# Performance work log

Hardware: AMD Instinct MI355X
Metric: run time of the kernel (lower is better)

Reference implementation:

```python
import jax, jax.numpy as jnp
import numpy as np

TK = 3          # number of temporal scales (wavedec level = TK-1)
SK = 3          # spatial rank count per scale (SK-1 rank-1 terms + residual)
INPUT_LEN = 256
N_NODES = 256
K = 32          # randomized-SVD sketch size
INV_SQRT2 = np.float32(1.0 / np.sqrt(2.0))


def haar_wavedec(x, levels):
    # x: (..., L) with L divisible by 2**levels; pywt haar, mode='zero', even L
    # returns [cD1, cD2, ..., cD_levels, cA_levels]  (== pywt.wavedec(...)[::-1])
    coeffs = []
    for _ in range(levels):
        L = x.shape[-1]
        pairs = x.reshape(x.shape[:-1] + (L // 2, 2))
        a, b = pairs[..., 0], pairs[..., 1]
        coeffs.append((a - b) * INV_SQRT2)  # detail cD
        x = (a + b) * INV_SQRT2             # approx cA
    coeffs.append(x)
    return coeffs


def setup_inputs() -> dict:
    key = jax.random.key(0)
    kx, kp = jax.random.split(key)
    x = jax.random.normal(kx, (4, INPUT_LEN, 64, N_NODES), dtype=jnp.float32)
    p = jax.random.normal(kp, (N_NODES, K), dtype=jnp.float32)
    return {"x": x, "p": p}


def reference(x, p):
    # x: (B, T, c, n) -> permute(0,2,3,1) -> (B, c, n, T)
    xw = jnp.transpose(x, (0, 2, 3, 1))
    coeffs = haar_wavedec(xw, TK - 1)  # TK tensors (B, c, n, L_i)
    res = []
    for xi in coeffs:
        if SK == 1:
            res.append(xi)
            continue
        xt = jnp.transpose(xi, (0, 3, 1, 2))          # (B, L, c, n)
        z = xt @ p                                     # (B, L, c, k)
        q, _ = jnp.linalg.qr(z)                        # reduced: (B, L, c, k)
        y = jnp.einsum('blck,blcn->blkn', q, xt)       # (B, L, k, n)
        u, s, vh = jnp.linalg.svd(y, full_matrices=False)  # u:(B,L,k,k) s:(B,L,k) vh:(B,L,k,n)
        u = q @ u                                      # (B, L, c, k)
        # rank-1 terms s_j * u_j v_j^T for j < SK-1, vectorized over j
        terms = jnp.einsum('blcj,blj,bljn->jblcn',
                           u[..., :SK - 1], s[..., :SK - 1], vh[..., :SK - 1, :])
        terms = jnp.transpose(terms, (0, 1, 3, 4, 2))  # (SK-1, B, c, n, L)
        resid = xi - terms.sum(axis=0)
        for j in range(SK - 1):
            res.append(terms[j])
        res.append(resid)
    # left-pad last dim to INPUT_LEN, then stack -> (TK*SK, B, c, n, INPUT_LEN)
    res = [jnp.pad(r, ((0, 0), (0, 0), (0, 0), (INPUT_LEN - r.shape[-1], 0))) for r in res]
    return jnp.stack(res)
```

## Files before the change

### kernel.cpp

```cpp
#include <hip/hip_runtime.h>

#define IS2f 0.70710678118654752440f

#define WS_Z   0ul
#define WS_G   2097152ul
#define WS_H   3145728ul
#define WS_SU  4194304ul
#define WS_VV  4325376ul
#define WS_B   4849664ul

#define WSYNC() asm volatile("" ::: "memory")

__device__ __forceinline__ float frcp(float v){ return __builtin_amdgcn_rcpf(v); }
__device__ __forceinline__ float frsq(float v){ return __builtin_amdgcn_rsqf(v); }
__device__ __forceinline__ float fsq (float v){ return __builtin_amdgcn_sqrtf(v); }
__device__ __forceinline__ float readlane_f(float v, int sl){
  return __uint_as_float(__builtin_amdgcn_readlane(__float_as_uint(v), sl));
}

__device__ __forceinline__ void decode_pid(int pid, int& ci, int& b, int& l, int& L){
  if (pid < 512)      { ci = 0; b = pid >> 7; l = pid & 127; L = 128; }
  else if (pid < 768) { int q = pid - 512; ci = 1; b = q >> 6; l = q & 63; L = 64; }
  else                { int q = pid - 768; ci = 2; b = q >> 6; l = q & 63; L = 64; }
}
__device__ __forceinline__ int su_base(int ci){ return ci==0 ? 0 : (ci==1 ? 65536 : 98304); }
__device__ __forceinline__ int vv_base(int ci){ return ci==0 ? 0 : (ci==1 ? 262144 : 393216); }
__device__ __forceinline__ int tpp(int r, int m){ return (m==0) ? r  : (r+m)%31; }
__device__ __forceinline__ int tqq(int r, int m){ return (m==0) ? 31 : (r+31-m)%31; }

#define PTS 260

__global__ __launch_bounds__(512) void k_fact(const float* __restrict__ x,
                                              const float* __restrict__ p,
                                              float* __restrict__ ws, int storeB){
  __shared__ __align__(16) float Ms[64*256];
  __shared__ __align__(16) float Zs[64*32];
  __shared__ __align__(16) float Pt[32*PTS];
  __shared__ __align__(16) float Bn[32*PTS];

  int pid = blockIdx.x, tid = threadIdx.x;
  int ci,b,l,L; decode_pid(pid,ci,b,l,L);

  {
    const float4* p4 = (const float4*)p;
    #pragma unroll
    for (int e=0;e<4;++e){
      int idx = tid + 512*e;
      int n = idx >> 3, k4 = idx & 7;
      float4 v = p4[idx];
      Pt[(4*k4+0)*PTS + n] = v.x;
      Pt[(4*k4+1)*PTS + n] = v.y;
      Pt[(4*k4+2)*PTS + n] = v.z;
      Pt[(4*k4+3)*PTS + n] = v.w;
    }
  }
  const float4* x4 = (const float4*)x;
  float4* Ms4 = (float4*)Ms;
  if (ci == 0){
    size_t base = ((size_t)(b*256 + 2*l) * 64) * 64;
    #pragma unroll
    for (int e=0;e<8;++e){
      int f = tid + 512*e;
      float4 A = x4[base + f];
      float4 Bv = x4[base + 4096 + f];
      float4 m;
      m.x=(A.x-Bv.x)*IS2f; m.y=(A.y-Bv.y)*IS2f; m.z=(A.z-Bv.z)*IS2f; m.w=(A.w-Bv.w)*IS2f;
      Ms4[f] = m;
    }
  } else {
    float sg = (ci==1) ? -0.5f : 0.5f;
    size_t base = ((size_t)(b*256 + 4*l) * 64) * 64;
    #pragma unroll
    for (int e=0;e<8;++e){
      int f = tid + 512*e;
      float4 A = x4[base + f];
      float4 B1 = x4[base + 4096 + f];
      float4 C1 = x4[base + 8192 + f];
      float4 D1 = x4[base + 12288 + f];
      float4 m;
      m.x=(A.x+B1.x)*0.5f + (C1.x+D1.x)*sg;
      m.y=(A.y+B1.y)*0.5f + (C1.y+D1.y)*sg;
      m.z=(A.z+B1.z)*0.5f + (C1.z+D1.z)*sg;
      m.w=(A.w+B1.w)*0.5f + (C1.w+D1.w)*sg;
      Ms4[f] = m;
    }
  }
  __syncthreads();

  {
    int k = tid & 31, c0 = tid >> 5;
    float acc[4] = {0,0,0,0};
    for (int n4=0;n4<64;++n4){
      float4 pv = *(const float4*)&Pt[k*PTS + 4*n4];
      #pragma unroll
      for (int i=0;i<4;++i){
        float4 m = Ms4[(c0*4+i)*64 + n4];
        acc[i] += m.x*pv.x + m.y*pv.y + m.z*pv.z + m.w*pv.w;
      }
    }
    #pragma unroll
    for (int i=0;i<4;++i){
      int c = c0*4 + i;
      Zs[c*32+k] = acc[i];
      ws[WS_Z + (size_t)pid*2048 + c*32 + k] = acc[i];
    }
  }
  __syncthreads();

  {
    int kk = tid & 31, j0 = tid >> 5;
    float ga[2] = {0,0};
    for (int c=0;c<64;++c){
      float zk = Zs[c*32+kk];
      #pragma unroll
      for (int e=0;e<2;++e) ga[e] += Zs[c*32 + j0 + 16*e] * zk;
    }
    #pragma unroll
    for (int e=0;e<2;++e)
      ws[WS_G + (size_t)pid*1024 + (j0+16*e)*32 + kk] = ga[e];
  }

  {
    int n4 = tid & 63, kg = tid >> 6;
    float4 facc[4];
    #pragma unroll
    for (int kq=0;kq<4;++kq){ facc[kq].x=0.f; facc[kq].y=0.f; facc[kq].z=0.f; facc[kq].w=0.f; }
    for (int c=0;c<64;++c){
      float4 mv = Ms4[c*64 + n4];
      float4 z1 = *(const float4*)&Zs[c*32 + kg*4];
      float zz[4] = {z1.x,z1.y,z1.z,z1.w};
      #pragma unroll
      for (int kq=0;kq<4;++kq){
        facc[kq].x += zz[kq]*mv.x; facc[kq].y += zz[kq]*mv.y;
        facc[kq].z += zz[kq]*mv.z; facc[kq].w += zz[kq]*mv.w;
      }
    }
    #pragma unroll
    for (int kq=0;kq<4;++kq){
      int krow = kg*4 + kq;
      *(float4*)&Bn[krow*PTS + 4*n4] = facc[kq];
      if (storeB)
        *(float4*)&ws[WS_B + (size_t)pid*8192 + (size_t)krow*256 + 4*n4] = facc[kq];
    }
  }
  __syncthreads();

  {
    int kk = tid & 31, j0 = tid >> 5;
    float h[2] = {0,0};
    for (int n4=0;n4<64;++n4){
      float4 bk = *(const float4*)&Bn[kk*PTS + 4*n4];
      #pragma unroll
      for (int e=0;e<2;++e){
        float4 bj = *(const float4*)&Bn[(j0+16*e)*PTS + 4*n4];
        h[e] += bj.x*bk.x + bj.y*bk.y + bj.z*bk.z + bj.w*bk.w;
      }
    }
    #pragma unroll
    for (int e=0;e<2;++e)
      ws[WS_H + (size_t)pid*1024 + (j0+16*e)*32 + kk] = h[e];
  }
}

#define NSWEEP 5

__global__ __launch_bounds__(128) void k_solve(const float* __restrict__ x,
                                               float* __restrict__ ws, int useB){
  __shared__ float Gs[32*33];
  __shared__ float Hs[32*33];
  __shared__ float Vsh[32*33];
  __shared__ float cA[16], sA[16];
  __shared__ float ggs[2][32];
  __shared__ float uss[2][64];

  int pid = blockIdx.x, tid = threadIdx.x;
  int wave = tid >> 6;
  int lane = tid & 63;
  int jlane = tid & 31;
  int wv4  = tid >> 5;
  int hlf  = (tid >> 5) & 1;
  int ci,b,l,L; decode_pid(pid,ci,b,l,L);

  #pragma unroll
  for (int e=0;e<8;++e){
    int idx = tid + 128*e; int i = idx>>5, j = idx&31;
    Gs[i*33+j]  = ws[WS_G + (size_t)pid*1024 + idx];
    Hs[i*33+j]  = ws[WS_H + (size_t)pid*1024 + idx];
    Vsh[i*33+j] = (i==j) ? 1.f : 0.f;
  }
  __syncthreads();

  for (int k=0;k<32;++k){
    float gkk  = Gs[k*33+k];
    float ginv = frcp(gkk);
    float gkj  = Gs[k*33+jlane];
    float av[8], bv[8];
    #pragma unroll
    for (int e=0;e<8;++e){
      int i = k+1+wv4+4*e; int ii = (i<32)? i : 31;
      av[e] = Gs[ii*33+jlane];
      bv[e] = Gs[k*33+ii];
    }
    WSYNC();
    #pragma unroll
    for (int e=0;e<8;++e){
      int i = k+1+wv4+4*e;
      if (i < 32) Gs[i*33+jlane] = av[e] - bv[e]*gkj*ginv;
    }
    __syncthreads();
  }
  {
    float sv[8];
    #pragma unroll
    for (int e=0;e<8;++e){
      int i = wv4+4*e;
      float d = Gs[i*33+i];
      sv[e] = Gs[i*33+jlane] * frsq(d);
    }
    WSYNC();
    #pragma unroll
    for (int e=0;e<8;++e){
      int i = wv4+4*e;
      Gs[i*33+jlane] = sv[e];
    }
  }
  __syncthreads();

  for (int i=0;i<32;++i){
    float rinv = frcp(Gs[i*33+i]);
    float hs   = Hs[i*33+jlane] * rinv;
    float av[8], bv[8];
    #pragma unroll
    for (int e=0;e<8;++e){
      int m = i+1+wv4+4*e; int mm = (m<32)? m : 31;
      av[e] = Hs[mm*33+jlane];
      bv[e] = Gs[i*33+mm];
    }
    WSYNC();
    #pragma unroll
    for (int e=0;e<8;++e){
      int m = i+1+wv4+4*e;
      if (m < 32) Hs[m*33+jlane] = av[e] - bv[e]*hs;
    }
    __syncthreads();
  }
  {
    float sv[8];
    #pragma unroll
    for (int e=0;e<8;++e){
      int m = wv4+4*e;
      sv[e] = Hs[m*33+jlane] * frcp(Gs[m*33+m]);
    }
    WSYNC();
    #pragma unroll
    for (int e=0;e<8;++e){
      int m = wv4+4*e;
      Hs[m*33+jlane] = sv[e];
    }
  }
  __syncthreads();

  for (int j=0;j<32;++j){
    float rinv = frcp(Gs[j*33+j]);
    float hs   = Hs[jlane*33+j] * rinv;
    float av[8], bv[8];
    #pragma unroll
    for (int e=0;e<8;++e){
      int m = j+1+wv4+4*e; int mm = (m<32)? m : 31;
      av[e] = Hs[jlane*33+mm];
      bv[e] = Gs[j*33+mm];
    }
    WSYNC();
    #pragma unroll
    for (int e=0;e<8;++e){
      int m = j+1+wv4+4*e;
      if (m < 32) Hs[jlane*33+m] = av[e] - bv[e]*hs;
    }
    __syncthreads();
  }
  {
    float sv[8];
    #pragma unroll
    for (int e=0;e<8;++e){
      int m = wv4+4*e;
      sv[e] = Hs[jlane*33+m] * frcp(Gs[m*33+m]);
    }
    WSYNC();
    #pragma unroll
    for (int e=0;e<8;++e){
      int m = wv4+4*e;
      Hs[jlane*33+m] = sv[e];
    }
  }
  __syncthreads();

  float dmx = (lane < 32) ? fabsf(Hs[jlane*33+jlane]) : 0.f;
  #pragma unroll
  for (int off=1; off<64; off<<=1) dmx = fmaxf(dmx, __shfl_xor(dmx, off));
  float thr = dmx * 3e-6f;

  for (int sw=0; sw<NSWEEP; ++sw){
    for (int r=0; r<31; ++r){
      if (wave == 0){
        int m = lane & 15;
        int pm = tpp(r,m), qm = tqq(r,m);
        float app = Hs[pm*33+pm];
        float aqq = Hs[qm*33+qm];
        float apq = Hs[pm*33+qm];
        if (!__ballot(fabsf(apq) > thr)) continue;
        float tau = (aqq - app) * frcp(2.f*apq);
        float tt  = ((tau>=0.f)?1.f:-1.f) * frcp(fabsf(tau) + fsq(fmaf(tau,tau,1.f)));
        float cc  = frsq(fmaf(tt,tt,1.f));
        float ss  = tt*cc;
        bool ok = fabsf(apq) > 1e-28f;
        if (lane < 16){ cA[lane] = ok?cc:1.f; sA[lane] = ok?ss:0.f; }
        WSYNC();

        int m2 = lane >> 2, lm = lane & 3;
        int p2 = tpp(r,m2), q2 = tqq(r,m2);
        float c2 = cA[m2], s2 = sA[m2];
        float a_[4], b_[4], c_[4], d_[4], c1v[4], s1v[4];
        int p1v[4], q1v[4];
        #pragma unroll
        for (int e=0;e<4;++e){
          int m1 = lm + 4*e;
          int p1 = tpp(r,m1), q1 = tqq(r,m1);
          p1v[e]=p1; q1v[e]=q1;
          c1v[e]=cA[m1]; s1v[e]=sA[m1];
          a_[e] = Hs[p1*33+p2]; b_[e] = Hs[p1*33+q2];
          c_[e] = Hs[q1*33+p2]; d_[e] = Hs[q1*33+q2];
        }
        WSYNC();
        #pragma unroll
        for (int e=0;e<4;++e){
          float c1 = c1v[e], s1 = s1v[e];
          float a1 = c1*a_[e] - s1*c_[e];
          float b1 = c1*b_[e] - s1*d_[e];
          float c1r= s1*a_[e] + c1*c_[e];
          float d1 = s1*b_[e] + c1*d_[e];
          Hs[p1v[e]*33+p2] = c2*a1 - s2*b1;
          Hs[p1v[e]*33+q2] = s2*a1 + c2*b1;
          Hs[q1v[e]*33+p2] = c2*c1r - s2*d1;
          Hs[q1v[e]*33+q2] = s2*c1r + c2*d1;
        }
      } else {
        int m2 = lane >> 2, lm = lane & 3;
        int p2 = tpp(r,m2), q2 = tqq(r,m2);
        float app = Hs[p2*33+p2];
        float aqq = Hs[q2*33+q2];
        float apq = Hs[p2*33+q2];
        if (!__ballot(fabsf(apq) > thr)) continue;
        float tau = (aqq - app) * frcp(2.f*apq);
        float tt  = ((tau>=0.f)?1.f:-1.f) * frcp(fabsf(tau) + fsq(fmaf(tau,tau,1.f)));
        float cc  = frsq(fmaf(tt,tt,1.f));
        float ss  = tt*cc;
        bool ok = fabsf(apq) > 1e-28f;
        float c2 = ok?cc:1.f, s2 = ok?ss:0.f;

        float vp[8], vq[8];
        #pragma unroll
        for (int e=0;e<8;++e){
          int i = lm + 4*e;
          vp[e] = Vsh[i*33+p2];
          vq[e] = Vsh[i*33+q2];
        }
        WSYNC();
        #pragma unroll
        for (int e=0;e<8;++e){
          int i = lm + 4*e;
          Vsh[i*33+p2] = c2*vp[e] - s2*vq[e];
          Vsh[i*33+q2] = s2*vp[e] + c2*vq[e];
        }
      }
      __syncthreads();
    }
  }
  __syncthreads();
  if (wave == 1) return;

  float rdgr = frcp(Gs[jlane*33+jlane]);

  float dv = (lane < 32) ? Hs[jlane*33+jlane] : -3e38f;
  float m1r = dv;
  #pragma unroll
  for (int off=1; off<64; off<<=1) m1r = fmaxf(m1r, __shfl_xor(m1r, off));
  unsigned long long bm = __ballot(dv == m1r);
  int i0 = __ffsll((unsigned long long)bm) - 1;
  float dv2 = (lane == i0) ? -3e38f : dv;
  float m2r = dv2;
  #pragma unroll
  for (int off=1; off<64; off<<=1) m2r = fmaxf(m2r, __shfl_xor(m2r, off));
  unsigned long long bm2 = __ballot(dv2 == m2r);
  int i1 = __ffsll((unsigned long long)bm2) - 1;

  float lam = hlf ? m2r : m1r;
  int   ti  = hlf ? i1 : i0;
  float sj  = fsq(fmaxf(lam, 0.f)); sj = fmaxf(sj, 1e-12f);
  float s0 = readlane_f(sj, 0);
  float s1 = readlane_f(sj, 32);

  {
    float rr = Vsh[jlane*33 + ti];
    float Greg[32];
    #pragma unroll
    for (int i=0;i<32;++i) Greg[i] = Gs[jlane*33+i];
    #pragma unroll
    for (int i=31;i>=0;--i){
      float ri = __shfl(rr,  hlf*32 + i);
      float di = __shfl(rdgr, i);
      float g  = ri * di;
      if (jlane == i) ggs[hlf][i] = g;
      if (jlane < i)  rr -= Greg[i]*g;
    }
  }
  WSYNC();

  {
    const float4* Z4 = (const float4*)(ws + WS_Z + (size_t)pid*2048);
    float u0 = 0.f, u1 = 0.f;
    #pragma unroll
    for (int k4=0;k4<8;++k4){
      float4 z = Z4[lane*8 + k4];
      u0 += z.x*ggs[0][k4*4+0] + z.y*ggs[0][k4*4+1] + z.z*ggs[0][k4*4+2] + z.w*ggs[0][k4*4+3];
      u1 += z.x*ggs[1][k4*4+0] + z.y*ggs[1][k4*4+1] + z.z*ggs[1][k4*4+2] + z.w*ggs[1][k4*4+3];
    }
    uss[0][lane] = u0; uss[1][lane] = u1;
    ws[WS_SU + su_base(ci) + ((size_t)(b*2+0)*64 + lane)*L + l] = s0*u0;
    ws[WS_SU + su_base(ci) + ((size_t)(b*2+1)*64 + lane)*L + l] = s1*u1;
  }
  WSYNC();

  float i0s = frcp(s0), i1s = frcp(s1);
  size_t vb0 = WS_VV + vv_base(ci) + ((size_t)(b*2+0)*L + l)*256 + lane*4;
  size_t vb1 = WS_VV + vv_base(ci) + ((size_t)(b*2+1)*L + l)*256 + lane*4;

  if (useB){
    const float4* B4 = (const float4*)(ws + WS_B + (size_t)pid*8192);
    float a0x=0,a0y=0,a0z=0,a0w=0, a1x=0,a1y=0,a1z=0,a1w=0;
    #pragma unroll 8
    for (int k=0;k<32;++k){
      float4 bv = B4[(size_t)k*64 + lane];
      float g0 = ggs[0][k], g1 = ggs[1][k];
      a0x += g0*bv.x; a0y += g0*bv.y; a0z += g0*bv.z; a0w += g0*bv.w;
      a1x += g1*bv.x; a1y += g1*bv.y; a1z += g1*bv.z; a1w += g1*bv.w;
    }
    float4 r0; r0.x=a0x*i0s; r0.y=a0y*i0s; r0.z=a0z*i0s; r0.w=a0w*i0s;
    float4 r1; r1.x=a1x*i1s; r1.y=a1y*i1s; r1.z=a1z*i1s; r1.w=a1w*i1s;
    *(float4*)(ws + vb0) = r0;
    *(float4*)(ws + vb1) = r1;
  } else {
    float a0x=0,a0y=0,a0z=0,a0w=0, a1x=0,a1y=0,a1z=0,a1w=0;
    const float4* x4 = (const float4*)x;
    if (ci == 0){
      size_t base = ((size_t)(b*256 + 2*l) * 64) * 64;
      #pragma unroll 2
      for (int c=0;c<64;++c){
        float4 A  = x4[base + c*64 + lane];
        float4 Bv = x4[base + 4096 + c*64 + lane];
        float mx=(A.x-Bv.x)*IS2f, my=(A.y-Bv.y)*IS2f, mz=(A.z-Bv.z)*IS2f, mw=(A.w-Bv.w)*IS2f;
        float uc0 = uss[0][c], uc1 = uss[1][c];
        a0x += uc0*mx; a0y += uc0*my; a0z += uc0*mz; a0w += uc0*mw;
        a1x += uc1*mx; a1y += uc1*my; a1z += uc1*mz; a1w += uc1*mw;
      }
    } else {
      float sg = (ci==1) ? -0.5f : 0.5f;
      size_t base = ((size_t)(b*256 + 4*l) * 64) * 64;
      #pragma unroll 2
      for (int c=0;c<64;++c){
        float4 A  = x4[base + c*64 + lane];
        float4 B1 = x4[base + 4096 + c*64 + lane];
        float4 C1 = x4[base + 8192 + c*64 + lane];
        float4 D1 = x4[base + 12288 + c*64 + lane];
        float mx=(A.x+B1.x)*0.5f + (C1.x+D1.x)*sg;
        float my=(A.y+B1.y)*0.5f + (C1.y+D1.y)*sg;
        float mz=(A.z+B1.z)*0.5f + (C1.z+D1.z)*sg;
        float mw=(A.w+B1.w)*0.5f + (C1.w+D1.w)*sg;
        float uc0 = uss[0][c], uc1 = uss[1][c];
        a0x += uc0*mx; a0y += uc0*my; a0z += uc0*mz; a0w += uc0*mw;
        a1x += uc1*mx; a1y += uc1*my; a1z += uc1*mz; a1w += uc1*mw;
      }
    }
    ws[vb0+0]=a0x*i0s; ws[vb0+1]=a0y*i0s; ws[vb0+2]=a0z*i0s; ws[vb0+3]=a0w*i0s;
    ws[vb1+0]=a1x*i1s; ws[vb1+1]=a1y*i1s; ws[vb1+2]=a1z*i1s; ws[vb1+3]=a1w*i1s;
  }
}

__global__ __launch_bounds__(256) void k_out(const float* __restrict__ x,
                                             const float* __restrict__ ws,
                                             float* __restrict__ out){
  __shared__ float d1[128*33];
  __shared__ float d2[64*33];
  __shared__ float a2s[64*33];
  __shared__ float Vs[2*128*33];
  __shared__ float Us[512];

  int nt = blockIdx.x, c = blockIdx.y, b = blockIdx.z;
  int n0 = nt * 32, tid = threadIdx.x;
  float* a1 = Vs;

  const float4* x4 = (const float4*)x;
  #pragma unroll
  for (int e=0;e<4;++e){
    int f = tid + 256*e; int l1 = f>>3, d4 = f&7;
    size_t r = ((size_t)(b*256 + 2*l1)*64 + c)*64 + (n0>>2) + d4;
    float4 A = x4[r], Bv = x4[r + 4096];
    int o = l1*33 + 4*d4;
    d1[o+0]=(A.x-Bv.x)*IS2f; d1[o+1]=(A.y-Bv.y)*IS2f; d1[o+2]=(A.z-Bv.z)*IS2f; d1[o+3]=(A.w-Bv.w)*IS2f;
    a1[o+0]=(A.x+Bv.x)*IS2f; a1[o+1]=(A.y+Bv.y)*IS2f; a1[o+2]=(A.z+Bv.z)*IS2f; a1[o+3]=(A.w+Bv.w)*IS2f;
  }
  __syncthreads();
  #pragma unroll
  for (int e=0;e<2;++e){
    int f = tid + 256*e; int l2 = f>>3, d4 = f&7;
    #pragma unroll
    for (int j=0;j<4;++j){
      int dn = 4*d4 + j;
      float aa = a1[(2*l2)*33 + dn], bb = a1[(2*l2+1)*33 + dn];
      d2[l2*33+dn]  = (aa-bb)*IS2f;
      a2s[l2*33+dn] = (aa+bb)*IS2f;
    }
  }
  #pragma unroll
  for (int e=0;e<2;++e){
    int idx = tid + 256*e;
    int j, l, L, so;
    if (idx < 256)      { j=idx>>7;        l=idx&127; L=128; so=0; }
    else if (idx < 384) { j=(idx-256)>>6;  l=idx&63;  L=64;  so=65536; }
    else                { j=(idx-384)>>6;  l=idx&63;  L=64;  so=98304; }
    Us[idx] = ws[WS_SU + so + ((size_t)(b*2+j)*64 + c)*L + l];
  }
  __syncthreads();

  for (int cc=0; cc<3; ++cc){
    int L   = (cc==0) ? 128 : 64;
    int pad = 256 - L;
    int sb  = cc*3;
    int uo  = (cc==0) ? 0 : (cc==1) ? 256 : 384;
    const float* cf = (cc==0) ? d1 : (cc==1) ? d2 : a2s;

    int iters = (2*L*32) >> 8;
    for (int e=0;e<iters;++e){
      int idx = tid + 256*e;
      int j = (idx >= L*32) ? 1 : 0;
      int rem = idx - j*L*32;
      int ll = rem >> 5, dn = rem & 31;
      Vs[j*4224 + ll*33 + dn] =
        ws[WS_VV + vv_base(cc) + ((size_t)(b*2+j)*L + ll)*256 + n0 + dn];
    }
    __syncthreads();

    int l = tid - pad;
    bool inr = (l >= 0);
    size_t obase = (size_t)sb*16777216 + (size_t)b*4194304 + (size_t)c*65536
                 + (size_t)n0*256 + tid;
    #pragma unroll 4
    for (int dn=0; dn<32; ++dn){
      float v0 = 0.f, v1 = 0.f, rv = 0.f;
      if (inr){
        float q0 = Us[uo + l]     * Vs[l*33 + dn];
        float q1 = Us[uo + L + l] * Vs[4224 + l*33 + dn];
        v0 = q0; v1 = q1;
        rv = cf[l*33 + dn] - q0 - q1;
      }
      out[obase + dn*256]            = v0;
      out[obase + dn*256 + 16777216] = v1;
      out[obase + dn*256 + 33554432] = rv;
    }
    __syncthreads();
  }
}

extern "C" void kernel_launch(void* const* d_in, const int* in_sizes, int n_in,
                              void* d_out, int out_size, void* d_ws, size_t ws_size,
                              hipStream_t stream) {
  const float* x = (const float*)d_in[0];
  const float* p = (const float*)d_in[1];
  float* out = (float*)d_out;
  float* ws  = (float*)d_ws;

  int useB = (ws_size >= (size_t)(WS_B + 1024ull*8192ull) * 4ull) ? 1 : 0;

  k_fact <<<1024, 512, 0, stream>>>(x, p, ws, useB);
  k_solve<<<1024, 128, 0, stream>>>(x, ws, useB);
  k_out  <<<dim3(8,64,4), 256, 0, stream>>>(x, ws, out);
}
```

Baseline: 452.6 us.

## Move Cholesky into factor kernel and form whitened B before Gram

The Cholesky factorization of the Gram matrix Z^T Z moves from the small solve kernel into the 512-thread factor kernel. Each of 256 threads then forward-substitutes its column of B by R^T, so the H Gram is computed from the orthonormalized rows and the solve kernel no longer does the two triangular solves on H. This removes about 96 sequential barrier-bound steps from the 128-thread solve kernel. In exchange the factor kernel gains 32 barrier steps, a register-heavy 32-element per-thread triangular solve, and extra shared memory.

Result: no change. 448.1 us (-1.0%).

```diff
diff --git a/kernel.cpp b/kernel.cpp
--- a/kernel.cpp
+++ b/kernel.cpp
@@ -37,6 +37,7 @@
   __shared__ __align__(16) float Zs[64*32];
   __shared__ __align__(16) float Pt[32*PTS];
   __shared__ __align__(16) float Bn[32*PTS];
+  __shared__ float Gl[33*33];
 
   int pid = blockIdx.x, tid = threadIdx.x;
   int ci,b,l,L; decode_pid(pid,ci,b,l,L);
@@ -117,7 +118,7 @@
     }
     #pragma unroll
     for (int e=0;e<2;++e)
-      ws[WS_G + (size_t)pid*1024 + (j0+16*e)*32 + kk] = ga[e];
+      Gl[(j0+16*e)*33 + kk] = ga[e];
   }
 
   {
@@ -142,6 +143,63 @@
       if (storeB)
         *(float4*)&ws[WS_B + (size_t)pid*8192 + (size_t)krow*256 + 4*n4] = facc[kq];
     }
+  }
+  __syncthreads();
+
+  {
+    int jlane = tid & 31, grp = tid >> 5;
+    for (int k=0;k<32;++k){
+      float gkk  = Gl[k*33+k];
+      float ginv = frcp(gkk);
+      float gkj  = Gl[k*33+jlane];
+      float av[2], bv[2];
+      #pragma unroll
+      for (int e=0;e<2;++e){
+        int i = k+1+grp+16*e; int ii = (i<32)? i : 31;
+        av[e] = Gl[ii*33+jlane];
+        bv[e] = Gl[k*33+ii];
+      }
+      WSYNC();
+      #pragma unroll
+      for (int e=0;e<2;++e){
+        int i = k+1+grp+16*e;
+        if (i < 32) Gl[i*33+jlane] = av[e] - bv[e]*gkj*ginv;
+      }
+      __syncthreads();
+    }
+    float sv[2];
+    #pragma unroll
+    for (int e=0;e<2;++e){
+      int i = grp+16*e;
+      sv[e] = Gl[i*33+jlane] * frsq(Gl[i*33+i]);
+    }
+    WSYNC();
+    #pragma unroll
+    for (int e=0;e<2;++e){
+      int i = grp+16*e;
+      Gl[i*33+jlane] = sv[e];
+    }
+  }
+  __syncthreads();
+
+  #pragma unroll
+  for (int e=0;e<2;++e){
+    int idx = tid + 512*e;
+    ws[WS_G + (size_t)pid*1024 + idx] = Gl[(idx>>5)*33 + (idx&31)];
+  }
+
+  if (tid < 256){
+    int n = tid;
+    float c[32];
+    #pragma unroll
+    for (int i=0;i<32;++i){
+      float cv = Bn[i*PTS + n];
+      #pragma unroll
+      for (int k=0;k<i;++k) cv -= Gl[k*33+i]*c[k];
+      c[i] = cv * frcp(Gl[i*33+i]);
+    }
+    #pragma unroll
+    for (int i=0;i<32;++i) Bn[i*PTS + n] = c[i];
   }
   __syncthreads();
 
@@ -177,7 +235,6 @@
   int wave = tid >> 6;
   int lane = tid & 63;
   int jlane = tid & 31;
-  int wv4  = tid >> 5;
   int hlf  = (tid >> 5) & 1;
   int ci,b,l,L; decode_pid(pid,ci,b,l,L);
 
@@ -187,110 +244,6 @@
     Gs[i*33+j]  = ws[WS_G + (size_t)pid*1024 + idx];
     Hs[i*33+j]  = ws[WS_H + (size_t)pid*1024 + idx];
     Vsh[i*33+j] = (i==j) ? 1.f : 0.f;
-  }
-  __syncthreads();
-
-  for (int k=0;k<32;++k){
-    float gkk  = Gs[k*33+k];
-    float ginv = frcp(gkk);
-    float gkj  = Gs[k*33+jlane];
-    float av[8], bv[8];
-    #pragma unroll
-    for (int e=0;e<8;++e){
-      int i = k+1+wv4+4*e; int ii = (i<32)? i : 31;
-      av[e] = Gs[ii*33+jlane];
-      bv[e] = Gs[k*33+ii];
-    }
-    WSYNC();
-    #pragma unroll
-    for (int e=0;e<8;++e){
-      int i = k+1+wv4+4*e;
-      if (i < 32) Gs[i*33+jlane] = av[e] - bv[e]*gkj*ginv;
-    }
-    __syncthreads();
-  }
-  {
-    float sv[8];
-    #pragma unroll
-    for (int e=0;e<8;++e){
-      int i = wv4+4*e;
-      float d = Gs[i*33+i];
-      sv[e] = Gs[i*33+jlane] * frsq(d);
-    }
-    WSYNC();
-    #pragma unroll
-    for (int e=0;e<8;++e){
-      int i = wv4+4*e;
-      Gs[i*33+jlane] = sv[e];
-    }
-  }
-  __syncthreads();
-
-  for (int i=0;i<32;++i){
-    float rinv = frcp(Gs[i*33+i]);
-    float hs   = Hs[i*33+jlane] * rinv;
-    float av[8], bv[8];
-    #pragma unroll
-    for (int e=0;e<8;++e){
-      int m = i+1+wv4+4*e; int mm = (m<32)? m : 31;
-      av[e] = Hs[mm*33+jlane];
-      bv[e] = Gs[i*33+mm];
-    }
-    WSYNC();
-    #pragma unroll
-    for (int e=0;e<8;++e){
-      int m = i+1+wv4+4*e;
-      if (m < 32) Hs[m*33+jlane] = av[e] - bv[e]*hs;
-    }
-    __syncthreads();
-  }
-  {
-    float sv[8];
-    #pragma unroll
-    for (int e=0;e<8;++e){
-      int m = wv4+4*e;
-      sv[e] = Hs[m*33+jlane] * frcp(Gs[m*33+m]);
-    }
-    WSYNC();
-    #pragma unroll
-    for (int e=0;e<8;++e){
-      int m = wv4+4*e;
-      Hs[m*33+jlane] = sv[e];
-    }
-  }
-  __syncthreads();
-
-  for (int j=0;j<32;++j){
-    float rinv = frcp(Gs[j*33+j]);
-    float hs   = Hs[jlane*33+j] * rinv;
-    float av[8], bv[8];
-    #pragma unroll
-    for (int e=0;e<8;++e){
-      int m = j+1+wv4+4*e; int mm = (m<32)? m : 31;
-      av[e] = Hs[jlane*33+mm];
-      bv[e] = Gs[j*33+mm];
-    }
-    WSYNC();
-    #pragma unroll
-    for (int e=0;e<8;++e){
-      int m = j+1+wv4+4*e;
-      if (m < 32) Hs[jlane*33+m] = av[e] - bv[e]*hs;
-    }
-    __syncthreads();
-  }
-  {
-    float sv[8];
-    #pragma unroll
-    for (int e=0;e<8;++e){
-      int m = wv4+4*e;
-      sv[e] = Hs[jlane*33+m] * frcp(Gs[m*33+m]);
-    }
-    WSYNC();
-    #pragma unroll
-    for (int e=0;e<8;++e){
-      int m = wv4+4*e;
-      Hs[jlane*33+m] = sv[e];
-    }
   }
   __syncthreads();
 
```
